# Kernel tuning notes

Hardware: AMD Instinct MI355X
Metric: run time of the kernel (lower is better)

## Reference

```python
import jax, jax.numpy as jnp
import numpy as np

B, C, ELL, EQ, E = 1024, 128, 16, 3, 10
P3, P2, P1 = 23, 5, 1


def setup_inputs() -> dict:
    key = jax.random.key(0)
    ks = jax.random.split(key, 8)
    x = jax.random.normal(ks[0], (B, C, ELL), dtype=jnp.float32)
    # element one-hot encoding
    elem = jax.random.randint(ks[1], (B,), 0, E)
    y = jax.nn.one_hot(elem, E, dtype=jnp.float32)
    # U matrices are fixed CG-coefficient tensors (constants); random stand-ins with correct shapes
    U3 = jax.random.normal(ks[2], (EQ, ELL, ELL, ELL, P3), dtype=jnp.float32) * 0.1
    U2 = jax.random.normal(ks[3], (EQ, ELL, ELL, P2), dtype=jnp.float32) * 0.1
    U1 = jax.random.normal(ks[4], (EQ, ELL, P1), dtype=jnp.float32) * 0.1
    # learned per-element weights, init stddev 1/num_params as in the module
    w_max = jax.random.normal(ks[5], (E, P3, C), dtype=jnp.float32) / P3
    w2 = jax.random.normal(ks[6], (E, P2, C), dtype=jnp.float32) / P2
    w1 = jax.random.normal(ks[7], (E, P1, C), dtype=jnp.float32) / P1
    return {"x": x, "y": y, "U3": U3, "U2": U2, "U1": U1,
            "w_max": w_max, "w2": w2, "w1": w1}


def reference(x, y, U3, U2, U1, w_max, w2, w1):
    # per-node element weight gather (y is one-hot over elements)
    wn3 = jnp.einsum('be,ekc->bkc', y, w_max)  # (B, P3, C)
    # main contraction: 'wxvik,ekc,bci,be->bcwxv', ordered to keep intermediates small
    t = jnp.einsum('bkc,bci->bcik', wn3, x)      # (B, C, ELL, P3)
    out = jnp.einsum('wxvik,bcik->bcwxv', U3, t)  # (B, C, EQ, ELL, ELL)
    # nu = 2 step
    wn2 = jnp.einsum('be,ekc->bkc', y, w2)
    c2 = jnp.einsum('wxvk,bkc->bcwxv', U2, wn2) + out
    out = jnp.einsum('bcwxi,bci->bcwx', c2, x)    # (B, C, EQ, ELL)
    # nu = 1 step
    wn1 = jnp.einsum('be,ekc->bkc', y, w1)
    c1 = jnp.einsum('wxk,bkc->bcwx', U1, wn1) + out
    out = jnp.einsum('bcwi,bci->bcw', c1, x)      # (B, C, EQ)
    return out.reshape(out.shape[0], -1)          # (B, C*EQ)
```

## Files before the change

### kernel.cpp

```cpp
#include <hip/hip_runtime.h>

#define B_    1024
#define C_    128
#define ELL   16
#define EQ    3
#define E_    10
#define P3    23
#define P2    5
#define NSEG  176
#define RSTR  180
#define SRS   (48 * RSTR)
#define KD    28

#define WS_CNT   0
#define WS_LIST  64
#define WS_S     65536

#define SEG_OFF_INIT {0,20,36,52,68,84,96,108,120,132,140,148,156,164,168,172}

__device__ void do_lists(const float* __restrict__ y, int* __restrict__ cnt_g,
                         int* __restrict__ list_g, int t) {
    __shared__ int lcnt[E_];
    if (t < E_) lcnt[t] = 0;
    __syncthreads();
    for (int r = 0; r < 4; ++r) {
        int b = t + 256 * r;
        int e = 0;
        #pragma unroll
        for (int j = 1; j < E_; ++j)
            if (y[b * E_ + j] > 0.5f) e = j;
        int slot = atomicAdd(&lcnt[e], 1);
        list_g[e * B_ + slot] = b;
    }
    __syncthreads();
    if (t < E_) {
        int c0 = lcnt[t];
        cnt_g[t] = c0;
        int last = (c0 > 0) ? list_g[t * B_ + c0 - 1] : 0;
        int cp = (c0 + 63) & ~63;
        if (cp > B_) cp = B_;
        for (int s2 = c0; s2 < cp; ++s2) list_g[t * B_ + s2] = last;
    }
}

__global__ __launch_bounds__(256, 2) void k_s(const float* __restrict__ U3,
                                              const float* __restrict__ U2,
                                              const float* __restrict__ wmax,
                                              const float* __restrict__ w2,
                                              const float* __restrict__ y,
                                              float* __restrict__ Sg,
                                              int* __restrict__ cnt_g,
                                              int* __restrict__ list_g) {
    const int t = threadIdx.x;
    if (blockIdx.x == 48) {
        if (blockIdx.y == 0 && blockIdx.z == 0) do_lists(y, cnt_g, list_g, t);
        return;
    }
    __shared__ __align__(16) float U3L[ELL * ELL * P3];
    __shared__ __align__(16) float wsm[KD * 32];

    const int j  = blockIdx.x;
    const int e  = blockIdx.y;
    const int cq = blockIdx.z;

    {
        const float4* src4 = (const float4*)(U3 + (size_t)j * (ELL * ELL * P3));
        float4* dst4 = (float4*)U3L;
        for (int f = t; f < 1472; f += 256) dst4[f] = src4[f];
    }
    for (int idx = t; idx < KD * 32; idx += 256) {
        int k = idx >> 5, cc = idx & 31, c = cq * 32 + cc;
        wsm[idx] = (k < 23) ? wmax[(e * P3 + k) * C_ + c]
                            : w2[(e * P2 + (k - 23)) * C_ + c];
    }
    __syncthreads();

    if (t >= NSEG) return;

    const int SO[16] = SEG_OFF_INIT;
    int v = 0;
    #pragma unroll
    for (int s = 1; s < 16; ++s) v += (t >= SO[s]) ? 1 : 0;
    const int l    = t - SO[v];
    const int real = 17 - v;

    float sk[P3], skl[P2];
    #pragma unroll
    for (int k = 0; k < P3; ++k) sk[k] = 0.f;
    #pragma unroll
    for (int q = 0; q < P2; ++q) skl[q] = 0.f;

    if (l == 0) {
        #pragma unroll
        for (int q = 0; q < P2; ++q)
            skl[q] = U2[(size_t)j * (ELL * P2) + v * P2 + q];
    } else if (l < real) {
        int i = v + l - 1;
        const float* pa = &U3L[(v * ELL + i) * P3];
        const float* pb = &U3L[(i * ELL + v) * P3];
        if (i != v) {
            #pragma unroll
            for (int k = 0; k < P3; ++k) sk[k] = pa[k] + pb[k];
        } else {
            #pragma unroll
            for (int k = 0; k < P3; ++k) sk[k] = pa[k];
        }
    }

    #pragma unroll
    for (int g = 0; g < 8; ++g) {
        float a[4] = {0.f, 0.f, 0.f, 0.f};
        #pragma unroll
        for (int k = 0; k < P3; ++k) {
            float4 wk = *(const float4*)&wsm[k * 32 + 4 * g];
            a[0] += sk[k] * wk.x; a[1] += sk[k] * wk.y;
            a[2] += sk[k] * wk.z; a[3] += sk[k] * wk.w;
        }
        #pragma unroll
        for (int q = 0; q < P2; ++q) {
            float4 wk = *(const float4*)&wsm[(23 + q) * 32 + 4 * g];
            a[0] += skl[q] * wk.x; a[1] += skl[q] * wk.y;
            a[2] += skl[q] * wk.z; a[3] += skl[q] * wk.w;
        }
        #pragma unroll
        for (int q2 = 0; q2 < 4; ++q2) {
            int c = cq * 32 + g * 4 + q2;
            Sg[(size_t)(e * C_ + c) * SRS + j * RSTR + t] = a[q2];
        }
    }
}

__global__ __launch_bounds__(256, 2) void k_main(
    const float* __restrict__ x, const float* __restrict__ Sg,
    const float* __restrict__ U1, const float* __restrict__ w1,
    const int* __restrict__ cnt_g, const int* __restrict__ list_g,
    float* __restrict__ out) {

    __shared__ __align__(16) float V3L[16 * RSTR];

    const int t  = threadIdx.x;
    const int bx = blockIdx.x;
    const int w  = bx % 3, c = bx / 3;
    const int e  = blockIdx.y;
    const int xx = t & 15, bs = t >> 4;
    const int cnt  = cnt_g[e];
    const int cntp = (cnt + 63) & ~63;

    {
        const float4* src = (const float4*)(Sg + (size_t)(e * C_ + c) * SRS
                                            + (size_t)w * 16 * RSTR);
        float4* dst = (float4*)V3L;
        #pragma unroll
        for (int r = 0; r < 2; ++r) dst[t + 256 * r] = src[t + 256 * r];
        if (t < 208) dst[512 + t] = src[512 + t];
    }
    const float v1x = U1[w * 16 + xx] * w1[e * C_ + c];
    __syncthreads();

    const float* v3p = &V3L[xx * RSTR];
    const int SO[16] = SEG_OFF_INIT;

    #pragma clang loop unroll(disable)
    for (int base = 0; base < cntp; base += 64) {
        __syncthreads();

        const int slot = base + bs * 4;
        int bidx[4];
        #pragma unroll
        for (int r = 0; r < 4; ++r) bidx[r] = list_g[e * B_ + slot + r];

        float xm[4][19];
        float xo[4];
        #pragma unroll
        for (int r = 0; r < 4; ++r) {
            const float* xb = x + ((size_t)bidx[r] * C_ + c) * ELL;
            #pragma unroll
            for (int i4 = 0; i4 < 4; ++i4) {
                float4 a = ((const float4*)xb)[i4];
                xm[r][4 * i4 + 0] = a.x; xm[r][4 * i4 + 1] = a.y;
                xm[r][4 * i4 + 2] = a.z; xm[r][4 * i4 + 3] = a.w;
            }
            xm[r][16] = 0.f; xm[r][17] = 0.f; xm[r][18] = 0.f;
            xo[r] = xb[xx];
        }

        float t2[4] = {0.f, 0.f, 0.f, 0.f};
        #pragma unroll
        for (int v = 0; v < 16; ++v) {
            const int off = SO[v];
            const int nf4 = (v == 0) ? 5 : (v < 5) ? 4 : (v < 9) ? 3 : (v < 13) ? 2 : 1;
            float inner[4];
            {
                float4 u = *(const float4*)(v3p + off);
                #pragma unroll
                for (int r = 0; r < 4; ++r)
                    inner[r] = u.x + u.y * xm[r][v]
                             + u.z * xm[r][v + 1] + u.w * xm[r][v + 2];
            }
            #pragma unroll
            for (int q = 1; q < nf4; ++q) {
                float4 u = *(const float4*)(v3p + off + 4 * q);
                #pragma unroll
                for (int r = 0; r < 4; ++r) {
                    inner[r] += u.x * xm[r][v + 4 * q - 1];
                    inner[r] += u.y * xm[r][v + 4 * q + 0];
                    inner[r] += u.z * xm[r][v + 4 * q + 1];
                    inner[r] += u.w * xm[r][v + 4 * q + 2];
                }
            }
            #pragma unroll
            for (int r = 0; r < 4; ++r) t2[r] += xm[r][v] * inner[r];
        }

        float cv[4];
        #pragma unroll
        for (int r = 0; r < 4; ++r) cv[r] = (t2[r] + v1x) * xo[r];
        #pragma unroll
        for (int m = 1; m < 16; m <<= 1) {
            #pragma unroll
            for (int r = 0; r < 4; ++r) cv[r] += __shfl_xor(cv[r], m, 16);
        }
        if (xx == 0) {
            #pragma unroll
            for (int r = 0; r < 4; ++r)
                if (slot + r < cnt)
                    out[(size_t)bidx[r] * (C_ * EQ) + c * EQ + w] = cv[r];
        }
    }
}

extern "C" void kernel_launch(void* const* d_in, const int* in_sizes, int n_in,
                              void* d_out, int out_size, void* d_ws, size_t ws_size,
                              hipStream_t stream) {
    const float* x    = (const float*)d_in[0];
    const float* y    = (const float*)d_in[1];
    const float* U3   = (const float*)d_in[2];
    const float* U2   = (const float*)d_in[3];
    const float* U1   = (const float*)d_in[4];
    const float* wmax = (const float*)d_in[5];
    const float* w2   = (const float*)d_in[6];
    const float* w1   = (const float*)d_in[7];
    float* out = (float*)d_out;
    char*  ws  = (char*)d_ws;

    int*   cnt_g  = (int*)(ws + WS_CNT);
    int*   list_g = (int*)(ws + WS_LIST);
    float* Sg     = (float*)(ws + WS_S);
    (void)ws_size;

    k_s<<<dim3(49, E_, 4), 256, 0, stream>>>(U3, U2, wmax, w2, y, Sg, cnt_g, list_g);
    k_main<<<dim3(C_ * EQ, E_), 256, 0, stream>>>(x, Sg, U1, w1, cnt_g, list_g, out);
}
```

Measured before the change: 138.8 us.

## Split coefficient precompute into separate kernel and use coalesced channel-major S layout

Coefficient symmetrization of U3/U2 now runs once per j in a new k_coef kernel, instead of once for every element and channel-quarter block. A new k_s kernel computes S with one channel per thread and writes float4 values interleaved by channel, so stores are coalesced. k_main gathers its S tile from this strided layout into shared memory. This removes redundant U3 loads and the scattered scalar stores of the old k_s, at the cost of one extra kernel launch and strided reads in k_main's prologue.

```diff
diff --git a/kernel.cpp b/kernel.cpp
--- a/kernel.cpp
+++ b/kernel.cpp
@@ -8,13 +8,14 @@
 #define P3    23
 #define P2    5
 #define NSEG  176
+#define NI4   44
 #define RSTR  180
-#define SRS   (48 * RSTR)
 #define KD    28
 
 #define WS_CNT   0
 #define WS_LIST  64
-#define WS_S     65536
+#define WS_COEF  65536
+#define WS_S     (2u << 20)
 
 #define SEG_OFF_INIT {0,20,36,52,68,84,96,108,120,132,140,148,156,164,168,172}
 
@@ -43,38 +44,23 @@
     }
 }
 
-__global__ __launch_bounds__(256, 2) void k_s(const float* __restrict__ U3,
-                                              const float* __restrict__ U2,
-                                              const float* __restrict__ wmax,
-                                              const float* __restrict__ w2,
-                                              const float* __restrict__ y,
-                                              float* __restrict__ Sg,
-                                              int* __restrict__ cnt_g,
-                                              int* __restrict__ list_g) {
+__global__ __launch_bounds__(256, 2) void k_coef(const float* __restrict__ U3,
+                                                 const float* __restrict__ U2,
+                                                 const float* __restrict__ y,
+                                                 float* __restrict__ coefG,
+                                                 int* __restrict__ cnt_g,
+                                                 int* __restrict__ list_g) {
     const int t = threadIdx.x;
-    if (blockIdx.x == 48) {
-        if (blockIdx.y == 0 && blockIdx.z == 0) do_lists(y, cnt_g, list_g, t);
-        return;
-    }
+    if (blockIdx.x == 48) { do_lists(y, cnt_g, list_g, t); return; }
     __shared__ __align__(16) float U3L[ELL * ELL * P3];
-    __shared__ __align__(16) float wsm[KD * 32];
-
-    const int j  = blockIdx.x;
-    const int e  = blockIdx.y;
-    const int cq = blockIdx.z;
+    const int j = blockIdx.x;
 
     {
         const float4* src4 = (const float4*)(U3 + (size_t)j * (ELL * ELL * P3));
         float4* dst4 = (float4*)U3L;
         for (int f = t; f < 1472; f += 256) dst4[f] = src4[f];
     }
-    for (int idx = t; idx < KD * 32; idx += 256) {
-        int k = idx >> 5, cc = idx & 31, c = cq * 32 + cc;
-        wsm[idx] = (k < 23) ? wmax[(e * P3 + k) * C_ + c]
-                            : w2[(e * P2 + (k - 23)) * C_ + c];
-    }
-    __syncthreads();
-
+    __syncthreads();
     if (t >= NSEG) return;
 
     const int SO[16] = SEG_OFF_INIT;
@@ -84,54 +70,67 @@
     const int l    = t - SO[v];
     const int real = 17 - v;
 
-    float sk[P3], skl[P2];
-    #pragma unroll
-    for (int k = 0; k < P3; ++k) sk[k] = 0.f;
-    #pragma unroll
-    for (int q = 0; q < P2; ++q) skl[q] = 0.f;
+    float outk[KD];
+    #pragma unroll
+    for (int k = 0; k < KD; ++k) outk[k] = 0.f;
 
     if (l == 0) {
         #pragma unroll
         for (int q = 0; q < P2; ++q)
-            skl[q] = U2[(size_t)j * (ELL * P2) + v * P2 + q];
+            outk[23 + q] = U2[(size_t)j * (ELL * P2) + v * P2 + q];
     } else if (l < real) {
         int i = v + l - 1;
         const float* pa = &U3L[(v * ELL + i) * P3];
         const float* pb = &U3L[(i * ELL + v) * P3];
         if (i != v) {
             #pragma unroll
-            for (int k = 0; k < P3; ++k) sk[k] = pa[k] + pb[k];
+            for (int k = 0; k < P3; ++k) outk[k] = pa[k] + pb[k];
         } else {
             #pragma unroll
-            for (int k = 0; k < P3; ++k) sk[k] = pa[k];
-        }
-    }
-
-    #pragma unroll
-    for (int g = 0; g < 8; ++g) {
-        float a[4] = {0.f, 0.f, 0.f, 0.f};
-        #pragma unroll
-        for (int k = 0; k < P3; ++k) {
-            float4 wk = *(const float4*)&wsm[k * 32 + 4 * g];
-            a[0] += sk[k] * wk.x; a[1] += sk[k] * wk.y;
-            a[2] += sk[k] * wk.z; a[3] += sk[k] * wk.w;
-        }
-        #pragma unroll
-        for (int q = 0; q < P2; ++q) {
-            float4 wk = *(const float4*)&wsm[(23 + q) * 32 + 4 * g];
-            a[0] += skl[q] * wk.x; a[1] += skl[q] * wk.y;
-            a[2] += skl[q] * wk.z; a[3] += skl[q] * wk.w;
-        }
-        #pragma unroll
-        for (int q2 = 0; q2 < 4; ++q2) {
-            int c = cq * 32 + g * 4 + q2;
-            Sg[(size_t)(e * C_ + c) * SRS + j * RSTR + t] = a[q2];
-        }
+            for (int k = 0; k < P3; ++k) outk[k] = pa[k];
+        }
+    }
+    float* cr = coefG + ((size_t)j * NSEG + t) * KD;
+    #pragma unroll
+    for (int k = 0; k < KD; ++k) cr[k] = outk[k];
+}
+
+__global__ __launch_bounds__(256, 4) void k_s(const float* __restrict__ coefG,
+                                              const float* __restrict__ wmax,
+                                              const float* __restrict__ w2,
+                                              float4* __restrict__ Sg4) {
+    const int t = threadIdx.x;
+    const int j = blockIdx.x, e = blockIdx.y;
+    const int c = t & 127, half = t >> 7;
+
+    float wl[KD];
+    #pragma unroll
+    for (int k = 0; k < P3; ++k) wl[k] = wmax[(e * P3 + k) * C_ + c];
+    #pragma unroll
+    for (int q = 0; q < P2; ++q) wl[23 + q] = w2[(e * P2 + q) * C_ + c];
+
+    const float* cb = coefG + (size_t)j * NSEG * KD;
+    float4* dst = Sg4 + (size_t)(e * 48 + j) * NI4 * 128 + c;
+
+    const int i4lo = half * 22, i4hi = i4lo + 22;
+    #pragma clang loop unroll(disable)
+    for (int i4 = i4lo; i4 < i4hi; ++i4) {
+        float s[4];
+        #pragma unroll
+        for (int l = 0; l < 4; ++l) {
+            const float* cr = cb + (size_t)(4 * i4 + l) * KD;
+            float a = 0.f;
+            #pragma unroll
+            for (int k = 0; k < KD; ++k) a += cr[k] * wl[k];
+            s[l] = a;
+        }
+        float4 o; o.x = s[0]; o.y = s[1]; o.z = s[2]; o.w = s[3];
+        dst[(size_t)i4 * 128] = o;
     }
 }
 
 __global__ __launch_bounds__(256, 2) void k_main(
-    const float* __restrict__ x, const float* __restrict__ Sg,
+    const float* __restrict__ x, const float4* __restrict__ Sg4,
     const float* __restrict__ U1, const float* __restrict__ w1,
     const int* __restrict__ cnt_g, const int* __restrict__ list_g,
     float* __restrict__ out) {
@@ -147,12 +146,16 @@
     const int cntp = (cnt + 63) & ~63;
 
     {
-        const float4* src = (const float4*)(Sg + (size_t)(e * C_ + c) * SRS
-                                            + (size_t)w * 16 * RSTR);
-        float4* dst = (float4*)V3L;
-        #pragma unroll
-        for (int r = 0; r < 2; ++r) dst[t + 256 * r] = src[t + 256 * r];
-        if (t < 208) dst[512 + t] = src[512 + t];
+        const float4* src = Sg4 + (size_t)(e * 48 + w * 16) * NI4 * 128 + c;
+        #pragma unroll
+        for (int rr = 0; rr < 3; ++rr) {
+            int f = t + 256 * rr;
+            if (f < 704) {
+                float4 u = src[(size_t)f * 128];
+                int row = f / NI4, i4 = f - row * NI4;
+                *(float4*)(&V3L[row * RSTR + 4 * i4]) = u;
+            }
+        }
     }
     const float v1x = U1[w * 16 + xx] * w1[e * C_ + c];
     __syncthreads();
@@ -243,11 +246,13 @@
     float* out = (float*)d_out;
     char*  ws  = (char*)d_ws;
 
-    int*   cnt_g  = (int*)(ws + WS_CNT);
-    int*   list_g = (int*)(ws + WS_LIST);
-    float* Sg     = (float*)(ws + WS_S);
+    int*    cnt_g  = (int*)(ws + WS_CNT);
+    int*    list_g = (int*)(ws + WS_LIST);
+    float*  coefG  = (float*)(ws + WS_COEF);
+    float4* Sg4    = (float4*)(ws + WS_S);
     (void)ws_size;
 
-    k_s<<<dim3(49, E_, 4), 256, 0, stream>>>(U3, U2, wmax, w2, y, Sg, cnt_g, list_g);
-    k_main<<<dim3(C_ * EQ, E_), 256, 0, stream>>>(x, Sg, U1, w1, cnt_g, list_g, out);
-}
+    k_coef<<<49, 256, 0, stream>>>(U3, U2, y, coefG, cnt_g, list_g);
+    k_s<<<dim3(48, E_), 256, 0, stream>>>(coefG, wmax, w2, Sg4);
+    k_main<<<dim3(C_ * EQ, E_), 256, 0, stream>>>(x, Sg4, U1, w1, cnt_g, list_g, out);
+}
```

Result: slower. 187.6 us (+35.2%).
